# Optimization experiments

Hardware: AMD Instinct MI355X
Metric: run time of the kernel (lower is better)

The kernel has to match this reference:

```python
import jax, jax.numpy as jnp
import numpy as np

C = 256; HEADS = 8; LEVELS = 4; POINTS = 4; D = C // HEADS
SPATIAL = np.array([[96, 96], [48, 48], [24, 24], [12, 12]], dtype=np.int32)  # (H, W) per level
AREAS = SPATIAL[:, 0] * SPATIAL[:, 1]
HW = int(AREAS.sum())  # 12240
LSI = np.concatenate([[0], np.cumsum(AREAS)[:-1]]).astype(np.int32)
N = 1; Q = HW


def setup_inputs() -> dict:
    key = jax.random.key(0)
    ks = jax.random.split(key, 12)
    s = 0.02
    return {
        "query": jax.random.normal(ks[0], (N, Q, C), jnp.float32),
        "reference_points": jax.random.uniform(ks[1], (N, Q, LEVELS, 2), jnp.float32),
        "input_flatten": jax.random.normal(ks[2], (N, HW, C), jnp.float32),
        "input_spatial_shapes": jnp.asarray(SPATIAL),
        "input_level_start_index": jnp.asarray(LSI),
        "W_off": jax.random.normal(ks[3], (C, HEADS * LEVELS * POINTS * 2), jnp.float32) * s,
        "b_off": jax.random.normal(ks[4], (HEADS * LEVELS * POINTS * 2,), jnp.float32) * s,
        "W_attn": jax.random.normal(ks[5], (C, HEADS * LEVELS * POINTS), jnp.float32) * s,
        "b_attn": jax.random.normal(ks[6], (HEADS * LEVELS * POINTS,), jnp.float32) * s,
        "W_val": jax.random.normal(ks[7], (C, C), jnp.float32) * (1.0 / np.sqrt(C)),
        "b_val": jax.random.normal(ks[8], (C,), jnp.float32) * s,
        "W_out": jax.random.normal(ks[9], (C, C), jnp.float32) * (1.0 / np.sqrt(C)),
        "b_out": jax.random.normal(ks[10], (C,), jnp.float32) * s,
    }


def _ms_deform_attn(query, reference_points, input_flatten, sp, lsi,
                    W_off, b_off, W_attn, b_attn, W_val, b_val, W_out, b_out):
    n, q, c = query.shape
    hw = input_flatten.shape[1]
    # value projection -> [N, Hd, HW, D]
    value = (input_flatten @ W_val + b_val).reshape(n, hw, HEADS, D).transpose(0, 2, 1, 3)
    # sampling offsets [N,Q,Hd,L,P,2]
    off = (query @ W_off + b_off).reshape(n, q, HEADS, LEVELS, POINTS, 2)
    # attention weights softmaxed over L*P (done inside the fused CUDA kernel)
    attn = jax.nn.softmax((query @ W_attn + b_attn).reshape(n, q, HEADS, LEVELS * POINTS), axis=-1)
    attn = attn.reshape(n, q, HEADS, LEVELS, POINTS)
    # normalized sampling locations (reference_points last dim == 2 branch)
    norm = jnp.stack([sp[:, 1], sp[:, 0]], -1).astype(query.dtype)  # (W, H) per level
    loc = reference_points[:, :, None, :, None, :] + off / norm[None, None, None, :, None, :]
    Hl = sp[:, 0][None, None, None, :, None]
    Wl = sp[:, 1][None, None, None, :, None]
    start = lsi[None, None, None, :, None]
    # grid_sample-style (align_corners=False) pixel coordinates
    x = loc[..., 0] * Wl - 0.5
    y = loc[..., 1] * Hl - 0.5
    x0 = jnp.floor(x); y0 = jnp.floor(y)
    lx = x - x0; ly = y - y0
    x0i = x0.astype(jnp.int32); y0i = y0.astype(jnp.int32)

    def gather(yi, xi):
        valid = (xi >= 0) & (xi < Wl) & (yi >= 0) & (yi < Hl)
        idx = jnp.where(valid, start + yi * Wl + xi, 0)  # [N,Q,Hd,L,P]
        idx_t = idx.transpose(0, 2, 1, 3, 4).reshape(n, HEADS, q * LEVELS * POINTS, 1)
        g = jnp.take_along_axis(value, idx_t, axis=2)  # [N,Hd,Q*L*P,D]
        g = g.reshape(n, HEADS, q, LEVELS, POINTS, D)
        return g * valid.transpose(0, 2, 1, 3, 4)[..., None]

    def w(a):
        return a.transpose(0, 2, 1, 3, 4)[..., None]  # [N,Hd,Q,L,P,1]

    sampled = (gather(y0i, x0i) * w((1 - ly) * (1 - lx))
               + gather(y0i, x0i + 1) * w((1 - ly) * lx)
               + gather(y0i + 1, x0i) * w(ly * (1 - lx))
               + gather(y0i + 1, x0i + 1) * w(ly * lx))  # [N,Hd,Q,L,P,D]
    out = jnp.einsum('nhqlpd,nqhlp->nqhd', sampled, attn).reshape(n, q, c)
    return out @ W_out + b_out


def reference(query, reference_points, input_flatten, input_spatial_shapes, input_level_start_index,
              W_off, b_off, W_attn, b_attn, W_val, b_val, W_out, b_out):
    return _ms_deform_attn(query, reference_points, input_flatten,
                           input_spatial_shapes, input_level_start_index,
                           W_off, b_off, W_attn, b_attn, W_val, b_val, W_out, b_out)
```

## Files before the change

kernel.cpp:

```cpp
#include <hip/hip_runtime.h>

#define QTOT 12240
#define KD   256

typedef float f32x4 __attribute__((ext_vector_type(4)));
typedef short s16x8 __attribute__((ext_vector_type(8)));
typedef unsigned short ushort_t;

__device__ __forceinline__ unsigned short f2b(float x) {
    union { float f; unsigned u; } c; c.f = x;
    unsigned r = c.u + 0x7fffu + ((c.u >> 16) & 1u);
    return (unsigned short)(r >> 16);
}
__device__ __forceinline__ int swz(int row, int kb) { return row * 512 + (kb ^ ((row & 7) << 4)); }

__global__ __launch_bounds__(256) void prep(
    const float* __restrict__ W_val, const float* __restrict__ W_off,
    const float* __restrict__ W_attn, const float* __restrict__ W_out,
    const float* __restrict__ b_off, const float* __restrict__ b_attn,
    ushort_t* __restrict__ WvT, ushort_t* __restrict__ WcT,
    ushort_t* __restrict__ WoT, float* __restrict__ bcomb)
{
    int id = blockIdx.x * 256 + threadIdx.x;
    if (id < 65536) { int n = id >> 8, k = id & 255; WvT[id] = f2b(W_val[k * 256 + n]); }
    else if (id < 163840) {
        int t = id - 65536; int n = t >> 8, k = t & 255;
        float v = (n < 256) ? W_off[k * 256 + n] : W_attn[k * 128 + (n - 256)];
        WcT[t] = f2b(v);
    } else if (id < 229376) {
        int t = id - 163840; int n = t >> 8, k = t & 255;
        WoT[t] = f2b(W_out[k * 256 + n]);
    } else if (id < 229760) {
        int t = id - 229376; bcomb[t] = (t < 256) ? b_off[t] : b_attn[t - 256];
    }
}

__global__ __launch_bounds__(256) void gemm1(
    const float* __restrict__ inflat, const float* __restrict__ query,
    const ushort_t* __restrict__ WvT, const ushort_t* __restrict__ WcT,
    const float* __restrict__ b_val, const float* __restrict__ bcomb,
    ushort_t* __restrict__ projb, ushort_t* __restrict__ offb,
    float* __restrict__ logitf)
{
    __shared__ char As[16384];
    const int b = blockIdx.x;
    const bool isval = b < 383;
    const int bm = (isval ? b : b - 383) * 32;
    const float* A = isval ? inflat : query;
    const ushort_t* WT = isval ? WvT : WcT;
    const int nc = isval ? 4 : 6;

    const int tid = threadIdx.x, lane = tid & 63, wave = tid >> 6;
    const int lr = lane & 15, g8 = (lane >> 4) * 8;

    {
        const int row = tid >> 3, c0 = (tid & 7) * 32;
        const int grow = bm + row;
        if (grow < QTOT) {
            const float4* src = (const float4*)(A + (size_t)grow * KD + c0);
#pragma unroll
            for (int j = 0; j < 4; ++j) {
                float4 f0 = src[j * 2 + 0], f1 = src[j * 2 + 1];
                s16x8 v;
                v[0] = f2b(f0.x); v[1] = f2b(f0.y); v[2] = f2b(f0.z); v[3] = f2b(f0.w);
                v[4] = f2b(f1.x); v[5] = f2b(f1.y); v[6] = f2b(f1.z); v[7] = f2b(f1.w);
                *(s16x8*)(As + swz(row, (c0 + j * 8) * 2)) = v;
            }
        } else {
            s16x8 z = (s16x8)0;
#pragma unroll
            for (int j = 0; j < 4; ++j)
                *(s16x8*)(As + swz(row, (c0 + j * 8) * 2)) = z;
        }
    }
    __syncthreads();

    const int rg = (lane >> 4) * 4;

    for (int c = 0; c < nc; ++c) {
        const int col = c * 64 + wave * 16 + lr;
        s16x8 bfr[8];
        {
            const ushort_t* bp = WT + (size_t)col * KD + g8;
#pragma unroll
            for (int kc = 0; kc < 8; ++kc) bfr[kc] = *(const s16x8*)(bp + kc * 32);
        }
        f32x4 acc[2];
        acc[0] = (f32x4)0.f; acc[1] = (f32x4)0.f;
#pragma unroll
        for (int kc = 0; kc < 8; ++kc) {
            const int kb = (kc * 32 + g8) * 2;
            s16x8 a0 = *(const s16x8*)(As + swz(lr,      kb));
            s16x8 a1 = *(const s16x8*)(As + swz(16 + lr, kb));
            acc[0] = __builtin_amdgcn_mfma_f32_16x16x32_bf16(a0, bfr[kc], acc[0], 0, 0, 0);
            acc[1] = __builtin_amdgcn_mfma_f32_16x16x32_bf16(a1, bfr[kc], acc[1], 0, 0, 0);
        }
        const float bb = isval ? b_val[col] : bcomb[col];
#pragma unroll
        for (int mf = 0; mf < 2; ++mf)
#pragma unroll
            for (int rr = 0; rr < 4; ++rr) {
                const int row = bm + mf * 16 + rg + rr;
                if (row >= QTOT) continue;
                const float v = acc[mf][rr] + bb;
                if (isval)          projb[(size_t)row * 256 + col] = f2b(v);
                else if (col < 256) offb [(size_t)row * 256 + col] = f2b(v);
                else                logitf[(size_t)row * 128 + col - 256] = v;
            }
    }
}

__global__ __launch_bounds__(256) void gemm_o(
    const ushort_t* __restrict__ Ab, const ushort_t* __restrict__ WoT,
    const float* __restrict__ b_out, float* __restrict__ out)
{
    const int bm = blockIdx.x * 32;
    const int tid = threadIdx.x, lane = tid & 63, wave = tid >> 6;
    const int lr = lane & 15, g8 = (lane >> 4) * 8;
    const int rg = (lane >> 4) * 4;

    const ushort_t* ap0;
    const ushort_t* ap1;
    {
        int r0 = bm + lr;      if (r0 >= QTOT) r0 = QTOT - 1;
        int r1 = bm + 16 + lr; if (r1 >= QTOT) r1 = QTOT - 1;
        ap0 = Ab + (size_t)r0 * KD + g8;
        ap1 = Ab + (size_t)r1 * KD + g8;
    }

#pragma unroll
    for (int c = 0; c < 4; ++c) {
        const int col = c * 64 + wave * 16 + lr;
        s16x8 bfr[8];
        {
            const ushort_t* bp = WoT + (size_t)col * KD + g8;
#pragma unroll
            for (int kc = 0; kc < 8; ++kc) bfr[kc] = *(const s16x8*)(bp + kc * 32);
        }
        f32x4 acc[2];
        acc[0] = (f32x4)0.f; acc[1] = (f32x4)0.f;
#pragma unroll
        for (int kc = 0; kc < 8; ++kc) {
            s16x8 a0 = *(const s16x8*)(ap0 + kc * 32);
            s16x8 a1 = *(const s16x8*)(ap1 + kc * 32);
            acc[0] = __builtin_amdgcn_mfma_f32_16x16x32_bf16(a0, bfr[kc], acc[0], 0, 0, 0);
            acc[1] = __builtin_amdgcn_mfma_f32_16x16x32_bf16(a1, bfr[kc], acc[1], 0, 0, 0);
        }
        const float bb = b_out[col];
#pragma unroll
        for (int mf = 0; mf < 2; ++mf)
#pragma unroll
            for (int rr = 0; rr < 4; ++rr) {
                const int row = bm + mf * 16 + rg + rr;
                if (row < QTOT) out[(size_t)row * 256 + col] = acc[mf][rr] + bb;
            }
    }
}

__global__ __launch_bounds__(256) void sample4(
    const float* __restrict__ rp, const ushort_t* __restrict__ offb,
    const float* __restrict__ logitf, const ushort_t* __restrict__ projb,
    const int* __restrict__ sp, const int* __restrict__ lsi,
    ushort_t* __restrict__ outpre)
{
    const int bid = blockIdx.x;
    const int qpair = (bid & 7) * 765 + (bid >> 3);
    const int tid = threadIdx.x;
    const int qi = tid >> 7;
    const int q = qpair * 2 + qi;

    __shared__ int   s_idx[256][4];
    __shared__ float s_w[256][4];

    {
        const int t = tid & 127;
        const int l = (t >> 2) & 3;
        float logit = logitf[(size_t)q * 128 + t];
        float mx = logit;
#pragma unroll
        for (int d = 1; d < 16; d <<= 1) mx = fmaxf(mx, __shfl_xor(mx, d));
        float e = __expf(logit - mx);
        float s = e;
#pragma unroll
        for (int d = 1; d < 16; d <<= 1) s += __shfl_xor(s, d);
        const float aw = e / s;

        const unsigned opk = *(const unsigned*)&offb[(size_t)q * 256 + t * 2];
        const float ox = __uint_as_float(opk << 16);
        const float oy = __uint_as_float(opk & 0xffff0000u);

        const int Hl = sp[l * 2], Wl = sp[l * 2 + 1], st = lsi[l];
        const float rx = rp[((size_t)q * 4 + l) * 2 + 0];
        const float ry = rp[((size_t)q * 4 + l) * 2 + 1];

        const float x = rx * (float)Wl + ox - 0.5f;
        const float y = ry * (float)Hl + oy - 0.5f;
        const float xf = floorf(x), yf = floorf(y);
        const int x0 = (int)xf, y0 = (int)yf;
        const float lx = x - xf, ly = y - yf;

        const bool vx0 = (x0 >= 0) && (x0 < Wl);
        const bool vx1 = (x0 + 1 >= 0) && (x0 + 1 < Wl);
        const bool vy0 = (y0 >= 0) && (y0 < Hl);
        const bool vy1 = (y0 + 1 >= 0) && (y0 + 1 < Hl);

        s_w[tid][0] = (vx0 && vy0) ? aw * (1.f - ly) * (1.f - lx) : 0.f;
        s_w[tid][1] = (vx1 && vy0) ? aw * (1.f - ly) * lx         : 0.f;
        s_w[tid][2] = (vx0 && vy1) ? aw * ly * (1.f - lx)         : 0.f;
        s_w[tid][3] = (vx1 && vy1) ? aw * ly * lx                 : 0.f;
        s_idx[tid][0] = (vx0 && vy0) ? (st + y0 * Wl + x0) * 512           : 0;
        s_idx[tid][1] = (vx1 && vy0) ? (st + y0 * Wl + x0 + 1) * 512       : 0;
        s_idx[tid][2] = (vx0 && vy1) ? (st + (y0 + 1) * Wl + x0) * 512     : 0;
        s_idx[tid][3] = (vx1 && vy1) ? (st + (y0 + 1) * Wl + x0 + 1) * 512 : 0;
    }
    __syncthreads();

    const int tt = tid & 127;
    const int h = tt >> 4, qtr = (tt >> 2) & 3, c8 = tt & 3;
    const char* basec = (const char*)projb + (h * 32 + c8 * 8) * 2;

    float a0 = 0, a1 = 0, a2 = 0, a3 = 0, a4 = 0, a5 = 0, a6 = 0, a7 = 0;
#pragma unroll
    for (int p = 0; p < 4; ++p) {
        const int slot = qi * 128 + h * 16 + qtr * 4 + p;
        const int4   id4 = *(const int4*)s_idx[slot];
        const float4 w4  = *(const float4*)s_w[slot];
#pragma unroll
        for (int c = 0; c < 4; ++c) {
            const int   id = (c == 0) ? id4.x : (c == 1) ? id4.y : (c == 2) ? id4.z : id4.w;
            const float w  = (c == 0) ? w4.x  : (c == 1) ? w4.y  : (c == 2) ? w4.z  : w4.w;
            const uint4 v = *(const uint4*)(basec + id);
            a0 += w * __uint_as_float(v.x << 16);
            a1 += w * __uint_as_float(v.x & 0xffff0000u);
            a2 += w * __uint_as_float(v.y << 16);
            a3 += w * __uint_as_float(v.y & 0xffff0000u);
            a4 += w * __uint_as_float(v.z << 16);
            a5 += w * __uint_as_float(v.z & 0xffff0000u);
            a6 += w * __uint_as_float(v.w << 16);
            a7 += w * __uint_as_float(v.w & 0xffff0000u);
        }
    }
    a0 += __shfl_xor(a0, 4); a1 += __shfl_xor(a1, 4);
    a2 += __shfl_xor(a2, 4); a3 += __shfl_xor(a3, 4);
    a4 += __shfl_xor(a4, 4); a5 += __shfl_xor(a5, 4);
    a6 += __shfl_xor(a6, 4); a7 += __shfl_xor(a7, 4);
    a0 += __shfl_xor(a0, 8); a1 += __shfl_xor(a1, 8);
    a2 += __shfl_xor(a2, 8); a3 += __shfl_xor(a3, 8);
    a4 += __shfl_xor(a4, 8); a5 += __shfl_xor(a5, 8);
    a6 += __shfl_xor(a6, 8); a7 += __shfl_xor(a7, 8);

    if (qtr == 0) {
        uint4 o;
        o.x = (unsigned)f2b(a0) | ((unsigned)f2b(a1) << 16);
        o.y = (unsigned)f2b(a2) | ((unsigned)f2b(a3) << 16);
        o.z = (unsigned)f2b(a4) | ((unsigned)f2b(a5) << 16);
        o.w = (unsigned)f2b(a6) | ((unsigned)f2b(a7) << 16);
        *(uint4*)&outpre[(size_t)q * 256 + h * 32 + c8 * 8] = o;
    }
}

extern "C" void kernel_launch(void* const* d_in, const int* in_sizes, int n_in,
                              void* d_out, int out_size, void* d_ws, size_t ws_size,
                              hipStream_t stream) {
    const float* query  = (const float*)d_in[0];
    const float* rp     = (const float*)d_in[1];
    const float* inflat = (const float*)d_in[2];
    const int*   sp     = (const int*)d_in[3];
    const int*   lsi    = (const int*)d_in[4];
    const float* W_off  = (const float*)d_in[5];
    const float* b_off  = (const float*)d_in[6];
    const float* W_attn = (const float*)d_in[7];
    const float* b_attn = (const float*)d_in[8];
    const float* W_val  = (const float*)d_in[9];
    const float* b_val  = (const float*)d_in[10];
    const float* W_out  = (const float*)d_in[11];
    const float* b_out  = (const float*)d_in[12];
    float* out = (float*)d_out;

    char* ws = (char*)d_ws;
    ushort_t* projb  = (ushort_t*)ws; ws += (size_t)QTOT * 256 * 2;
    ushort_t* offb   = (ushort_t*)ws; ws += (size_t)QTOT * 256 * 2;
    float*    logitf = (float*)ws;    ws += (size_t)QTOT * 128 * 4;
    ushort_t* outpre = (ushort_t*)ws; ws += (size_t)QTOT * 256 * 2;
    ushort_t* WvT    = (ushort_t*)ws; ws += 65536 * 2;
    ushort_t* WcT    = (ushort_t*)ws; ws += 98304 * 2;
    ushort_t* WoT    = (ushort_t*)ws; ws += 65536 * 2;
    float*    bcomb  = (float*)ws;    ws += 384 * 4;

    dim3 blk(256);

    prep<<<dim3(898), blk, 0, stream>>>(W_val, W_off, W_attn, W_out, b_off, b_attn,
                                        WvT, WcT, WoT, bcomb);

    gemm1<<<dim3(766), blk, 0, stream>>>(inflat, query, WvT, WcT, b_val, bcomb,
                                         projb, offb, logitf);

    sample4<<<dim3(6120), blk, 0, stream>>>(rp, offb, logitf, projb, sp, lsi, outpre);

    gemm_o<<<dim3(383), blk, 0, stream>>>(outpre, WoT, b_out, out);
}
```

Before: 72.78 us.

## Fuse deformable sampling with output projection GEMM in one kernel

Merges the sampling kernel and the output projection GEMM into a single kernel. Each 512-thread block samples 32 queries in four sub-batches, stages the bf16 pre-projection rows in swizzled shared memory, then runs MFMA against W_out directly. This removes the outpre global round trip and one kernel launch. In exchange the grid drops from 6120 to 383 blocks, and each block uses much more shared memory (about 48KB), which may reduce occupancy and latency hiding for the gather loads.

```diff
diff --git a/kernel.cpp b/kernel.cpp
--- a/kernel.cpp
+++ b/kernel.cpp
@@ -110,152 +110,174 @@
     }
 }
 
-__global__ __launch_bounds__(256) void gemm_o(
-    const ushort_t* __restrict__ Ab, const ushort_t* __restrict__ WoT,
-    const float* __restrict__ b_out, float* __restrict__ out)
-{
-    const int bm = blockIdx.x * 32;
-    const int tid = threadIdx.x, lane = tid & 63, wave = tid >> 6;
-    const int lr = lane & 15, g8 = (lane >> 4) * 8;
-    const int rg = (lane >> 4) * 4;
-
-    const ushort_t* ap0;
-    const ushort_t* ap1;
-    {
-        int r0 = bm + lr;      if (r0 >= QTOT) r0 = QTOT - 1;
-        int r1 = bm + 16 + lr; if (r1 >= QTOT) r1 = QTOT - 1;
-        ap0 = Ab + (size_t)r0 * KD + g8;
-        ap1 = Ab + (size_t)r1 * KD + g8;
-    }
-
-#pragma unroll
-    for (int c = 0; c < 4; ++c) {
-        const int col = c * 64 + wave * 16 + lr;
-        s16x8 bfr[8];
-        {
-            const ushort_t* bp = WoT + (size_t)col * KD + g8;
-#pragma unroll
-            for (int kc = 0; kc < 8; ++kc) bfr[kc] = *(const s16x8*)(bp + kc * 32);
-        }
-        f32x4 acc[2];
-        acc[0] = (f32x4)0.f; acc[1] = (f32x4)0.f;
-#pragma unroll
-        for (int kc = 0; kc < 8; ++kc) {
-            s16x8 a0 = *(const s16x8*)(ap0 + kc * 32);
-            s16x8 a1 = *(const s16x8*)(ap1 + kc * 32);
-            acc[0] = __builtin_amdgcn_mfma_f32_16x16x32_bf16(a0, bfr[kc], acc[0], 0, 0, 0);
-            acc[1] = __builtin_amdgcn_mfma_f32_16x16x32_bf16(a1, bfr[kc], acc[1], 0, 0, 0);
-        }
-        const float bb = b_out[col];
-#pragma unroll
-        for (int mf = 0; mf < 2; ++mf)
-#pragma unroll
-            for (int rr = 0; rr < 4; ++rr) {
-                const int row = bm + mf * 16 + rg + rr;
-                if (row < QTOT) out[(size_t)row * 256 + col] = acc[mf][rr] + bb;
-            }
-    }
-}
-
-__global__ __launch_bounds__(256) void sample4(
+__global__ __launch_bounds__(512) void sample_o(
     const float* __restrict__ rp, const ushort_t* __restrict__ offb,
     const float* __restrict__ logitf, const ushort_t* __restrict__ projb,
     const int* __restrict__ sp, const int* __restrict__ lsi,
-    ushort_t* __restrict__ outpre)
+    const ushort_t* __restrict__ WoT, const float* __restrict__ b_out,
+    float* __restrict__ out)
 {
+    __shared__ int   s_idx[1024][4];
+    __shared__ float s_w[1024][4];
+    __shared__ char  outp[16384];
+
     const int bid = blockIdx.x;
-    const int qpair = (bid & 7) * 765 + (bid >> 3);
+    const int bm = bid * 32;
     const int tid = threadIdx.x;
-    const int qi = tid >> 7;
-    const int q = qpair * 2 + qi;
-
-    __shared__ int   s_idx[256][4];
-    __shared__ float s_w[256][4];
-
-    {
-        const int t = tid & 127;
-        const int l = (t >> 2) & 3;
-        float logit = logitf[(size_t)q * 128 + t];
-        float mx = logit;
-#pragma unroll
-        for (int d = 1; d < 16; d <<= 1) mx = fmaxf(mx, __shfl_xor(mx, d));
-        float e = __expf(logit - mx);
-        float s = e;
-#pragma unroll
-        for (int d = 1; d < 16; d <<= 1) s += __shfl_xor(s, d);
-        const float aw = e / s;
-
-        const unsigned opk = *(const unsigned*)&offb[(size_t)q * 256 + t * 2];
-        const float ox = __uint_as_float(opk << 16);
-        const float oy = __uint_as_float(opk & 0xffff0000u);
-
-        const int Hl = sp[l * 2], Wl = sp[l * 2 + 1], st = lsi[l];
-        const float rx = rp[((size_t)q * 4 + l) * 2 + 0];
-        const float ry = rp[((size_t)q * 4 + l) * 2 + 1];
-
-        const float x = rx * (float)Wl + ox - 0.5f;
-        const float y = ry * (float)Hl + oy - 0.5f;
-        const float xf = floorf(x), yf = floorf(y);
-        const int x0 = (int)xf, y0 = (int)yf;
-        const float lx = x - xf, ly = y - yf;
-
-        const bool vx0 = (x0 >= 0) && (x0 < Wl);
-        const bool vx1 = (x0 + 1 >= 0) && (x0 + 1 < Wl);
-        const bool vy0 = (y0 >= 0) && (y0 < Hl);
-        const bool vy1 = (y0 + 1 >= 0) && (y0 + 1 < Hl);
-
-        s_w[tid][0] = (vx0 && vy0) ? aw * (1.f - ly) * (1.f - lx) : 0.f;
-        s_w[tid][1] = (vx1 && vy0) ? aw * (1.f - ly) * lx         : 0.f;
-        s_w[tid][2] = (vx0 && vy1) ? aw * ly * (1.f - lx)         : 0.f;
-        s_w[tid][3] = (vx1 && vy1) ? aw * ly * lx                 : 0.f;
-        s_idx[tid][0] = (vx0 && vy0) ? (st + y0 * Wl + x0) * 512           : 0;
-        s_idx[tid][1] = (vx1 && vy0) ? (st + y0 * Wl + x0 + 1) * 512       : 0;
-        s_idx[tid][2] = (vx0 && vy1) ? (st + (y0 + 1) * Wl + x0) * 512     : 0;
-        s_idx[tid][3] = (vx1 && vy1) ? (st + (y0 + 1) * Wl + x0 + 1) * 512 : 0;
-    }
-    __syncthreads();
-
-    const int tt = tid & 127;
-    const int h = tt >> 4, qtr = (tt >> 2) & 3, c8 = tt & 3;
-    const char* basec = (const char*)projb + (h * 32 + c8 * 8) * 2;
-
-    float a0 = 0, a1 = 0, a2 = 0, a3 = 0, a4 = 0, a5 = 0, a6 = 0, a7 = 0;
-#pragma unroll
-    for (int p = 0; p < 4; ++p) {
-        const int slot = qi * 128 + h * 16 + qtr * 4 + p;
-        const int4   id4 = *(const int4*)s_idx[slot];
-        const float4 w4  = *(const float4*)s_w[slot];
-#pragma unroll
-        for (int c = 0; c < 4; ++c) {
-            const int   id = (c == 0) ? id4.x : (c == 1) ? id4.y : (c == 2) ? id4.z : id4.w;
-            const float w  = (c == 0) ? w4.x  : (c == 1) ? w4.y  : (c == 2) ? w4.z  : w4.w;
-            const uint4 v = *(const uint4*)(basec + id);
-            a0 += w * __uint_as_float(v.x << 16);
-            a1 += w * __uint_as_float(v.x & 0xffff0000u);
-            a2 += w * __uint_as_float(v.y << 16);
-            a3 += w * __uint_as_float(v.y & 0xffff0000u);
-            a4 += w * __uint_as_float(v.z << 16);
-            a5 += w * __uint_as_float(v.z & 0xffff0000u);
-            a6 += w * __uint_as_float(v.w << 16);
-            a7 += w * __uint_as_float(v.w & 0xffff0000u);
-        }
-    }
-    a0 += __shfl_xor(a0, 4); a1 += __shfl_xor(a1, 4);
-    a2 += __shfl_xor(a2, 4); a3 += __shfl_xor(a3, 4);
-    a4 += __shfl_xor(a4, 4); a5 += __shfl_xor(a5, 4);
-    a6 += __shfl_xor(a6, 4); a7 += __shfl_xor(a7, 4);
-    a0 += __shfl_xor(a0, 8); a1 += __shfl_xor(a1, 8);
-    a2 += __shfl_xor(a2, 8); a3 += __shfl_xor(a3, 8);
-    a4 += __shfl_xor(a4, 8); a5 += __shfl_xor(a5, 8);
-    a6 += __shfl_xor(a6, 8); a7 += __shfl_xor(a7, 8);
-
-    if (qtr == 0) {
-        uint4 o;
-        o.x = (unsigned)f2b(a0) | ((unsigned)f2b(a1) << 16);
-        o.y = (unsigned)f2b(a2) | ((unsigned)f2b(a3) << 16);
-        o.z = (unsigned)f2b(a4) | ((unsigned)f2b(a5) << 16);
-        o.w = (unsigned)f2b(a6) | ((unsigned)f2b(a7) << 16);
-        *(uint4*)&outpre[(size_t)q * 256 + h * 32 + c8 * 8] = o;
+
+    for (int sb = 0; sb < 4; ++sb) {
+        const int qloc0 = sb * 8;
+#pragma unroll
+        for (int rep = 0; rep < 2; ++rep) {
+            const int task = rep * 512 + tid;
+            const int ql = task >> 7, t = task & 127;
+            const int l = (t >> 2) & 3;
+            int q = bm + qloc0 + ql;
+            const int qc = (q < QTOT) ? q : (QTOT - 1);
+
+            float logit = logitf[(size_t)qc * 128 + t];
+            float mx = logit;
+#pragma unroll
+            for (int d = 1; d < 16; d <<= 1) mx = fmaxf(mx, __shfl_xor(mx, d));
+            float e = __expf(logit - mx);
+            float s = e;
+#pragma unroll
+            for (int d = 1; d < 16; d <<= 1) s += __shfl_xor(s, d);
+            const float aw = e / s;
+
+            const unsigned opk = *(const unsigned*)&offb[(size_t)qc * 256 + t * 2];
+            const float ox = __uint_as_float(opk << 16);
+            const float oy = __uint_as_float(opk & 0xffff0000u);
+
+            const int Hl = sp[l * 2], Wl = sp[l * 2 + 1], st = lsi[l];
+            const float rx = rp[((size_t)qc * 4 + l) * 2 + 0];
+            const float ry = rp[((size_t)qc * 4 + l) * 2 + 1];
+
+            const float x = rx * (float)Wl + ox - 0.5f;
+            const float y = ry * (float)Hl + oy - 0.5f;
+            const float xf = floorf(x), yf = floorf(y);
+            const int x0 = (int)xf, y0 = (int)yf;
+            const float lx = x - xf, ly = y - yf;
+
+            const bool vx0 = (x0 >= 0) && (x0 < Wl);
+            const bool vx1 = (x0 + 1 >= 0) && (x0 + 1 < Wl);
+            const bool vy0 = (y0 >= 0) && (y0 < Hl);
+            const bool vy1 = (y0 + 1 >= 0) && (y0 + 1 < Hl);
+
+            s_w[task][0] = (vx0 && vy0) ? aw * (1.f - ly) * (1.f - lx) : 0.f;
+            s_w[task][1] = (vx1 && vy0) ? aw * (1.f - ly) * lx         : 0.f;
+            s_w[task][2] = (vx0 && vy1) ? aw * ly * (1.f - lx)         : 0.f;
+            s_w[task][3] = (vx1 && vy1) ? aw * ly * lx                 : 0.f;
+            s_idx[task][0] = (vx0 && vy0) ? (st + y0 * Wl + x0) * 512           : 0;
+            s_idx[task][1] = (vx1 && vy0) ? (st + y0 * Wl + x0 + 1) * 512       : 0;
+            s_idx[task][2] = (vx0 && vy1) ? (st + (y0 + 1) * Wl + x0) * 512     : 0;
+            s_idx[task][3] = (vx1 && vy1) ? (st + (y0 + 1) * Wl + x0 + 1) * 512 : 0;
+        }
+        __syncthreads();
+
+        {
+            const int t = tid & 127, qlA = tid >> 7;
+            const int h = t >> 4, pq = (t >> 2) & 3, c8 = t & 3;
+            const char* basec = (const char*)projb + (h * 32 + c8 * 8) * 2;
+
+            float aA[8] = {0,0,0,0,0,0,0,0};
+            float aB[8] = {0,0,0,0,0,0,0,0};
+#pragma unroll
+            for (int l = 0; l < 4; ++l) {
+                const int slotA = (qlA << 7)       + h * 16 + l * 4 + pq;
+                const int slotB = ((qlA + 4) << 7) + h * 16 + l * 4 + pq;
+                const int4   iA = *(const int4*)s_idx[slotA];
+                const float4 wA = *(const float4*)s_w[slotA];
+                const int4   iB = *(const int4*)s_idx[slotB];
+                const float4 wB = *(const float4*)s_w[slotB];
+#pragma unroll
+                for (int c = 0; c < 4; ++c) {
+                    const int   idA = (c == 0) ? iA.x : (c == 1) ? iA.y : (c == 2) ? iA.z : iA.w;
+                    const float wwA = (c == 0) ? wA.x : (c == 1) ? wA.y : (c == 2) ? wA.z : wA.w;
+                    const uint4 v = *(const uint4*)(basec + idA);
+                    aA[0] += wwA * __uint_as_float(v.x << 16);
+                    aA[1] += wwA * __uint_as_float(v.x & 0xffff0000u);
+                    aA[2] += wwA * __uint_as_float(v.y << 16);
+                    aA[3] += wwA * __uint_as_float(v.y & 0xffff0000u);
+                    aA[4] += wwA * __uint_as_float(v.z << 16);
+                    aA[5] += wwA * __uint_as_float(v.z & 0xffff0000u);
+                    aA[6] += wwA * __uint_as_float(v.w << 16);
+                    aA[7] += wwA * __uint_as_float(v.w & 0xffff0000u);
+                }
+#pragma unroll
+                for (int c = 0; c < 4; ++c) {
+                    const int   idB = (c == 0) ? iB.x : (c == 1) ? iB.y : (c == 2) ? iB.z : iB.w;
+                    const float wwB = (c == 0) ? wB.x : (c == 1) ? wB.y : (c == 2) ? wB.z : wB.w;
+                    const uint4 v = *(const uint4*)(basec + idB);
+                    aB[0] += wwB * __uint_as_float(v.x << 16);
+                    aB[1] += wwB * __uint_as_float(v.x & 0xffff0000u);
+                    aB[2] += wwB * __uint_as_float(v.y << 16);
+                    aB[3] += wwB * __uint_as_float(v.y & 0xffff0000u);
+                    aB[4] += wwB * __uint_as_float(v.z << 16);
+                    aB[5] += wwB * __uint_as_float(v.z & 0xffff0000u);
+                    aB[6] += wwB * __uint_as_float(v.w << 16);
+                    aB[7] += wwB * __uint_as_float(v.w & 0xffff0000u);
+                }
+            }
+#pragma unroll
+            for (int i = 0; i < 8; ++i) {
+                aA[i] += __shfl_xor(aA[i], 4);  aA[i] += __shfl_xor(aA[i], 8);
+                aB[i] += __shfl_xor(aB[i], 4);  aB[i] += __shfl_xor(aB[i], 8);
+            }
+            if (pq == 0) {
+                const int colb = (h * 32 + c8 * 8) * 2;
+                uint4 o;
+                o.x = (unsigned)f2b(aA[0]) | ((unsigned)f2b(aA[1]) << 16);
+                o.y = (unsigned)f2b(aA[2]) | ((unsigned)f2b(aA[3]) << 16);
+                o.z = (unsigned)f2b(aA[4]) | ((unsigned)f2b(aA[5]) << 16);
+                o.w = (unsigned)f2b(aA[6]) | ((unsigned)f2b(aA[7]) << 16);
+                *(uint4*)(outp + swz(qloc0 + qlA, colb)) = o;
+                o.x = (unsigned)f2b(aB[0]) | ((unsigned)f2b(aB[1]) << 16);
+                o.y = (unsigned)f2b(aB[2]) | ((unsigned)f2b(aB[3]) << 16);
+                o.z = (unsigned)f2b(aB[4]) | ((unsigned)f2b(aB[5]) << 16);
+                o.w = (unsigned)f2b(aB[6]) | ((unsigned)f2b(aB[7]) << 16);
+                *(uint4*)(outp + swz(qloc0 + qlA + 4, colb)) = o;
+            }
+        }
+        __syncthreads();
+    }
+
+    const int lane = tid & 63, wave = tid >> 6;
+    const int lr = lane & 15, g8 = (lane >> 4) * 8, rg = (lane >> 4) * 4;
+
+    s16x8 bfr[2][8];
+#pragma unroll
+    for (int nf = 0; nf < 2; ++nf) {
+        const ushort_t* bp = WoT + (size_t)(wave * 32 + nf * 16 + lr) * KD + g8;
+#pragma unroll
+        for (int kc = 0; kc < 8; ++kc) bfr[nf][kc] = *(const s16x8*)(bp + kc * 32);
+    }
+
+    f32x4 acc[2][2];
+    acc[0][0] = (f32x4)0.f; acc[0][1] = (f32x4)0.f;
+    acc[1][0] = (f32x4)0.f; acc[1][1] = (f32x4)0.f;
+#pragma unroll
+    for (int kc = 0; kc < 8; ++kc) {
+        const int kb = (kc * 32 + g8) * 2;
+        s16x8 a0 = *(const s16x8*)(outp + swz(lr,      kb));
+        s16x8 a1 = *(const s16x8*)(outp + swz(16 + lr, kb));
+        acc[0][0] = __builtin_amdgcn_mfma_f32_16x16x32_bf16(a0, bfr[0][kc], acc[0][0], 0, 0, 0);
+        acc[1][0] = __builtin_amdgcn_mfma_f32_16x16x32_bf16(a1, bfr[0][kc], acc[1][0], 0, 0, 0);
+        acc[0][1] = __builtin_amdgcn_mfma_f32_16x16x32_bf16(a0, bfr[1][kc], acc[0][1], 0, 0, 0);
+        acc[1][1] = __builtin_amdgcn_mfma_f32_16x16x32_bf16(a1, bfr[1][kc], acc[1][1], 0, 0, 0);
+    }
+
+#pragma unroll
+    for (int nf = 0; nf < 2; ++nf) {
+        const int col = wave * 32 + nf * 16 + lr;
+        const float bb = b_out[col];
+#pragma unroll
+        for (int mf = 0; mf < 2; ++mf)
+#pragma unroll
+            for (int rr = 0; rr < 4; ++rr) {
+                const int row = bm + mf * 16 + rg + rr;
+                if (row < QTOT) out[(size_t)row * 256 + col] = acc[mf][nf][rr] + bb;
+            }
     }
 }
 
@@ -281,21 +303,17 @@
     ushort_t* projb  = (ushort_t*)ws; ws += (size_t)QTOT * 256 * 2;
     ushort_t* offb   = (ushort_t*)ws; ws += (size_t)QTOT * 256 * 2;
     float*    logitf = (float*)ws;    ws += (size_t)QTOT * 128 * 4;
-    ushort_t* outpre = (ushort_t*)ws; ws += (size_t)QTOT * 256 * 2;
     ushort_t* WvT    = (ushort_t*)ws; ws += 65536 * 2;
     ushort_t* WcT    = (ushort_t*)ws; ws += 98304 * 2;
     ushort_t* WoT    = (ushort_t*)ws; ws += 65536 * 2;
     float*    bcomb  = (float*)ws;    ws += 384 * 4;
 
-    dim3 blk(256);
-
-    prep<<<dim3(898), blk, 0, stream>>>(W_val, W_off, W_attn, W_out, b_off, b_attn,
-                                        WvT, WcT, WoT, bcomb);
-
-    gemm1<<<dim3(766), blk, 0, stream>>>(inflat, query, WvT, WcT, b_val, bcomb,
-                                         projb, offb, logitf);
-
-    sample4<<<dim3(6120), blk, 0, stream>>>(rp, offb, logitf, projb, sp, lsi, outpre);
-
-    gemm_o<<<dim3(383), blk, 0, stream>>>(outpre, WoT, b_out, out);
-}
+    prep<<<dim3(898), dim3(256), 0, stream>>>(W_val, W_off, W_attn, W_out, b_off, b_attn,
+                                              WvT, WcT, WoT, bcomb);
+
+    gemm1<<<dim3(766), dim3(256), 0, stream>>>(inflat, query, WvT, WcT, b_val, bcomb,
+                                               projb, offb, logitf);
+
+    sample_o<<<dim3(383), dim3(512), 0, stream>>>(rp, offb, logitf, projb, sp, lsi,
+                                                  WoT, b_out, out);
+}
```

Result: slower. 82.24 us (+13.0%).
